# Performance work log

Hardware: AMD Instinct MI355X
Metric: run time of the kernel (lower is better)

## Reference

```python
import jax, jax.numpy as jnp
import numpy as np

N = 100000
E = 1600000
EPS = 1e-5


def _bn(h, g, b):
    # BatchNorm1d in training mode: batch stats over dim 0 (biased variance)
    mu = h.mean(0)
    var = ((h - mu) ** 2).mean(0)
    return g * (h - mu) * jax.lax.rsqrt(var + EPS) + b


def setup_inputs() -> dict:
    key = jax.random.key(0)

    def nrm(i, shape, scale=1.0):
        return jax.random.normal(jax.random.fold_in(key, i), shape, jnp.float32) * scale

    inp = {
        "x": nrm(0, (N, 1)),
        "edge_attr": nrm(1, (E, 2)),
        "edge_index": jax.random.randint(jax.random.fold_in(key, 2), (2, E), 0, N),
        "dir_edge_index": jax.random.randint(jax.random.fold_in(key, 3), (2, E), 0, N),
        "prop_edge_index": jax.random.randint(jax.random.fold_in(key, 4), (2, E), 0, N),
    }
    k = [10]

    def lin(name, fan_in, fan_out):
        inp[name] = nrm(k[0], (fan_in, fan_out), 1.0 / float(np.sqrt(fan_in)))
        k[0] += 1

    def bnp(prefix, c):
        inp[prefix + "_g"] = jnp.ones((c,), jnp.float32)
        inp[prefix + "_b"] = jnp.zeros((c,), jnp.float32)

    lin("c1_ws", 1, 2); lin("c1_wn", 1, 2); lin("c1_we", 2, 2); bnp("c1", 2)
    lin("d1_ws", 3, 4); lin("d1_wn", 3, 4); bnp("d1", 4)
    lin("c2_ws", 5, 6); lin("c2_wn", 5, 6); lin("c2_we", 2, 6); bnp("c2", 6)
    lin("d2_ws", 7, 8); lin("d2_wn", 7, 8); bnp("d2", 8)
    lin("c3_ws", 9, 10); lin("c3_wn", 9, 10); lin("c3_we", 2, 10); bnp("c3", 10)
    lin("d3_ws", 11, 12); lin("d3_wn", 11, 12); bnp("d3", 12)
    lin("pw1", 13, 8); inp["pb1"] = jnp.zeros((8,), jnp.float32); bnp("p1", 8)
    lin("pw2", 8, 4); inp["pb2"] = jnp.zeros((4,), jnp.float32); bnp("p2", 4)
    lin("pw3", 4, 1); inp["pb3"] = jnp.zeros((1,), jnp.float32)
    lin("ew1", 28, 14); inp["eb1"] = jnp.zeros((14,), jnp.float32); bnp("e1", 14)
    lin("ew2", 14, 1); inp["eb2"] = jnp.zeros((1,), jnp.float32)
    return inp


def reference(x, edge_attr, edge_index, dir_edge_index, prop_edge_index,
              c1_ws, c1_wn, c1_we, c1_g, c1_b,
              d1_ws, d1_wn, d1_g, d1_b,
              c2_ws, c2_wn, c2_we, c2_g, c2_b,
              d2_ws, d2_wn, d2_g, d2_b,
              c3_ws, c3_wn, c3_we, c3_g, c3_b,
              d3_ws, d3_wn, d3_g, d3_b,
              pw1, pb1, p1_g, p1_b, pw2, pb2, p2_g, p2_b, pw3, pb3,
              ew1, eb1, e1_g, e1_b, ew2, eb2):
    n = x.shape[0]
    src, dst = edge_index[0], edge_index[1]        # x_j = x[src], x_i = x[dst]
    psrc, pdst = prop_edge_index[0], prop_edge_index[1]

    def flexconv(h, ws, wn, we, g, b):
        m = jax.nn.relu(_bn(h[dst] @ ws + edge_attr @ we + h[src] @ wn, g, b))
        agg = jax.ops.segment_sum(m, dst, num_segments=n)
        return jnp.concatenate([h[:, :1], agg], axis=1)

    def edgeinter(h, ws, wn, g, b):
        m = jax.nn.relu(_bn(h[pdst] @ ws + h[psrc] @ wn, g, b))
        agg = jax.ops.segment_sum(m, pdst, num_segments=n)
        return jnp.concatenate([h[:, :1], agg], axis=1)

    out = flexconv(x, c1_ws, c1_wn, c1_we, c1_g, c1_b)      # [N,3]
    out = edgeinter(out, d1_ws, d1_wn, d1_g, d1_b)          # [N,5]
    out = flexconv(out, c2_ws, c2_wn, c2_we, c2_g, c2_b)    # [N,7]
    out = edgeinter(out, d2_ws, d2_wn, d2_g, d2_b)          # [N,9]
    out = flexconv(out, c3_ws, c3_wn, c3_we, c3_g, c3_b)    # [N,11]
    out = edgeinter(out, d3_ws, d3_wn, d3_g, d3_b)          # [N,13]

    h = _bn(jax.nn.relu(out @ pw1 + pb1), p1_g, p1_b)
    h = _bn(jax.nn.relu(h @ pw2 + pb2), p2_g, p2_b)
    power = jax.nn.sigmoid(1.5 * (h @ pw3 + pb3))           # [N,1]

    dsrc, ddst = dir_edge_index[0], dir_edge_index[1]
    f = jnp.concatenate([out[ddst], power[ddst], out[dsrc], power[dsrc]], axis=1)  # [E,28]
    e = _bn(jax.nn.relu(f @ ew1 + eb1), e1_g, e1_b)
    direction = jax.nn.sigmoid(1.5 * (e @ ew2 + eb2))       # [E,1]
    return power, direction
```

## Files before the change

kernel.cpp:

```cpp
#include <hip/hip_runtime.h>
#include <math.h>

static constexpr int BLK = 256;
static constexpr float BN_EPS = 1e-5f;

__device__ __forceinline__ float sigmoid15(float z) {
    return 1.0f / (1.0f + expf(-1.5f * z));
}

template<int C>
__device__ __forceinline__ void block_stats_reduce(float (&s)[C], float (&ss)[C],
                                                   double* __restrict__ stats)
{
    #pragma unroll
    for (int j = 0; j < C; ++j) {
        #pragma unroll
        for (int o = 32; o > 0; o >>= 1) {
            s[j]  += __shfl_down(s[j],  o, 64);
            ss[j] += __shfl_down(ss[j], o, 64);
        }
    }
    __shared__ float red[2][C][BLK / 64];
    const int wave = threadIdx.x >> 6, lane = threadIdx.x & 63;
    if (lane == 0) {
        #pragma unroll
        for (int j = 0; j < C; ++j) { red[0][j][wave] = s[j]; red[1][j][wave] = ss[j]; }
    }
    __syncthreads();
    if (threadIdx.x < C) {
        const int j = threadIdx.x;
        float a = 0.f, b = 0.f;
        #pragma unroll
        for (int w = 0; w < BLK / 64; ++w) { a += red[0][j][w]; b += red[1][j][w]; }
        atomicAdd(&stats[j],      (double)a);
        atomicAdd(&stats[16 + j], (double)b);
    }
}

template<int C>
__device__ __forceinline__ void bn_coefs(const double* __restrict__ stats,
                                         const float* __restrict__ g, const float* __restrict__ b,
                                         double invE, float (&sc)[C], float (&bb)[C])
{
    #pragma unroll
    for (int j = 0; j < C; ++j) {
        const double mu  = stats[j] * invE;
        const double var = stats[16 + j] * invE - mu * mu;
        const float inv = rsqrtf((float)(var + (double)BN_EPS));
        const float gg = g[j];
        sc[j] = gg * inv;
        bb[j] = b[j] - (float)mu * gg * inv;
    }
}


__global__ __launch_bounds__(BLK) void init_kernel(int* __restrict__ deg, double* __restrict__ stats,
                                                   int* __restrict__ rowstart, int n2, int total)
{
    const int i = blockIdx.x * blockDim.x + threadIdx.x;
    if (i < n2) deg[i] = 0;
    if (i < 288) stats[i] = 0.0;
    if (i == 0) rowstart[n2] = total;
}

__global__ __launch_bounds__(BLK) void hist_kernel(const int* __restrict__ edst,
                                                   const int* __restrict__ pdst,
                                                   int* __restrict__ deg, int N, int E)
{
    const int stride = gridDim.x * blockDim.x;
    for (int e = blockIdx.x * blockDim.x + threadIdx.x; e < E; e += stride) {
        atomicAdd(&deg[edst[e]], 1);
        atomicAdd(&deg[N + pdst[e]], 1);
    }
}

__global__ __launch_bounds__(256) void scan1_kernel(const int* __restrict__ deg,
                                                    int* __restrict__ rowstart,
                                                    int* __restrict__ partials, int n2)
{
    __shared__ int lds[256];
    const int tid = threadIdx.x;
    const int base = blockIdx.x * 1024 + tid * 4;
    int v[4]; int loc = 0;
    #pragma unroll
    for (int r = 0; r < 4; ++r) { v[r] = (base + r < n2) ? deg[base + r] : 0; loc += v[r]; }
    lds[tid] = loc; __syncthreads();
    #pragma unroll
    for (int off = 1; off < 256; off <<= 1) {
        int t = (tid >= off) ? lds[tid - off] : 0;
        __syncthreads();
        lds[tid] += t;
        __syncthreads();
    }
    int excl = lds[tid] - loc;
    int run = excl;
    #pragma unroll
    for (int r = 0; r < 4; ++r) {
        if (base + r < n2) rowstart[base + r] = run;
        run += v[r];
    }
    if (tid == 255) partials[blockIdx.x] = lds[255];
}

__global__ __launch_bounds__(256) void scan2_kernel(int* __restrict__ partials, int n)
{
    __shared__ int lds[256];
    const int tid = threadIdx.x;
    const int base = tid * 4;
    int v[4]; int loc = 0;
    #pragma unroll
    for (int r = 0; r < 4; ++r) { v[r] = (base + r < n) ? partials[base + r] : 0; loc += v[r]; }
    lds[tid] = loc; __syncthreads();
    #pragma unroll
    for (int off = 1; off < 256; off <<= 1) {
        int t = (tid >= off) ? lds[tid - off] : 0;
        __syncthreads();
        lds[tid] += t;
        __syncthreads();
    }
    int excl = lds[tid] - loc;
    int run = excl;
    #pragma unroll
    for (int r = 0; r < 4; ++r) {
        if (base + r < n) partials[base + r] = run;
        run += v[r];
    }
}

__global__ __launch_bounds__(BLK) void scan3_kernel(int* __restrict__ rowstart,
                                                    int* __restrict__ cursor,
                                                    const int* __restrict__ partials, int n2)
{
    const int i = blockIdx.x * blockDim.x + threadIdx.x;
    if (i >= n2) return;
    const int v = rowstart[i] + partials[i >> 10];
    rowstart[i] = v;
    cursor[i] = v;
}

__global__ __launch_bounds__(BLK) void fill_kernel(
    const int* __restrict__ esrc, const int* __restrict__ edst,
    const int* __restrict__ psrc, const int* __restrict__ pdst,
    const float* __restrict__ ea,
    int* __restrict__ cursor, unsigned int* __restrict__ csr_src,
    float2* __restrict__ csr_ea, int N, int E)
{
    const int stride = gridDim.x * blockDim.x;
    for (int e = blockIdx.x * blockDim.x + threadIdx.x; e < E; e += stride) {
        const int d = edst[e];
        const int pos = atomicAdd(&cursor[d], 1);
        csr_src[pos] = (unsigned int)esrc[e];
        csr_ea[pos] = ((const float2*)ea)[e];
        const int p = pdst[e];
        const int pos2 = atomicAdd(&cursor[N + p], 1);
        csr_src[pos2] = (unsigned int)psrc[e];
    }
}


template<int CIN, int COUT>
__global__ __launch_bounds__(BLK) void projQ_kernel(
    const float* __restrict__ x, const float* __restrict__ agg_in,
    const float* __restrict__ wn, float* __restrict__ Q, int n)
{
    constexpr int PAD = (COUT + 3) & ~3;
    __shared__ float swn[CIN * COUT];
    for (int i = threadIdx.x; i < CIN * COUT; i += blockDim.x) swn[i] = wn[i];
    __syncthreads();
    const int i = blockIdx.x * blockDim.x + threadIdx.x;
    if (i >= n) return;
    float h[CIN];
    h[0] = x[i];
    #pragma unroll
    for (int k = 1; k < CIN; ++k) h[k] = agg_in[(size_t)i * (CIN - 1) + (k - 1)];
    #pragma unroll
    for (int j = 0; j < COUT; ++j) {
        float q = 0.f;
        #pragma unroll
        for (int k = 0; k < CIN; ++k) q = fmaf(h[k], swn[k * COUT + j], q);
        Q[(size_t)i * PAD + j] = q;
    }
}

template<int CIN, int COUT, bool HASEA>
__global__ __launch_bounds__(BLK) void node_stats_kernel(
    const int* __restrict__ rowstart, const unsigned int* __restrict__ csr_src,
    const float2* __restrict__ csr_ea,
    const float* __restrict__ x, const float* __restrict__ agg_in,
    const float* __restrict__ ws, const float* __restrict__ Q,
    const float* __restrict__ we,
    double* __restrict__ stats, int N, int base)
{
    constexpr int PAD = (COUT + 3) & ~3;
    __shared__ float sws[CIN * COUT];
    for (int i = threadIdx.x; i < CIN * COUT; i += blockDim.x) sws[i] = ws[i];
    __syncthreads();
    float we0[COUT], we1[COUT];
    if constexpr (HASEA) {
        #pragma unroll
        for (int j = 0; j < COUT; ++j) { we0[j] = we[j]; we1[j] = we[COUT + j]; }
    }
    float s[COUT], ss[COUT];
    #pragma unroll
    for (int j = 0; j < COUT; ++j) { s[j] = 0.f; ss[j] = 0.f; }
    const int t = blockIdx.x * blockDim.x + threadIdx.x;
    const int i = t >> 1, half = t & 1;
    if (i < N) {
        float h[CIN];
        h[0] = x[i];
        #pragma unroll
        for (int k = 1; k < CIN; ++k) h[k] = agg_in[(size_t)i * (CIN - 1) + (k - 1)];
        float pp[COUT];
        #pragma unroll
        for (int j = 0; j < COUT; ++j) {
            float p = 0.f;
            #pragma unroll
            for (int k = 0; k < CIN; ++k) p = fmaf(h[k], sws[k * COUT + j], p);
            pp[j] = p;
        }
        const int k0 = rowstart[base + i], k1 = rowstart[base + i + 1];
        for (int k = k0 + half; k < k1; k += 2) {
            const unsigned int sn = csr_src[k];
            float2 eav;
            if constexpr (HASEA) eav = csr_ea[k];
            #pragma unroll
            for (int j = 0; j < COUT; ++j) {
                float m = pp[j] + Q[(size_t)sn * PAD + j];
                if constexpr (HASEA) m = fmaf(eav.x, we0[j], fmaf(eav.y, we1[j], m));
                s[j] += m; ss[j] = fmaf(m, m, ss[j]);
            }
        }
    }
    block_stats_reduce<COUT>(s, ss, stats);
}

template<int CIN, int COUT, bool HASEA>
__global__ __launch_bounds__(BLK) void node_agg_kernel(
    const int* __restrict__ rowstart, const unsigned int* __restrict__ csr_src,
    const float2* __restrict__ csr_ea,
    const float* __restrict__ x, const float* __restrict__ agg_in,
    const float* __restrict__ ws, const float* __restrict__ Q,
    const float* __restrict__ we,
    const float* __restrict__ g, const float* __restrict__ b,
    const double* __restrict__ stats,
    float* __restrict__ agg_out, int N, int base, float invE)
{
    constexpr int PAD = (COUT + 3) & ~3;
    __shared__ float sws[CIN * COUT];
    for (int i = threadIdx.x; i < CIN * COUT; i += blockDim.x) sws[i] = ws[i];
    __syncthreads();
    const int t = blockIdx.x * blockDim.x + threadIdx.x;
    const int i = t >> 1, half = t & 1;
    if (i >= N) return;
    float we0[COUT], we1[COUT];
    if constexpr (HASEA) {
        #pragma unroll
        for (int j = 0; j < COUT; ++j) { we0[j] = we[j]; we1[j] = we[COUT + j]; }
    }
    float sc[COUT], bb[COUT];
    bn_coefs<COUT>(stats, g, b, (double)invE, sc, bb);
    float h[CIN];
    h[0] = x[i];
    #pragma unroll
    for (int k = 1; k < CIN; ++k) h[k] = agg_in[(size_t)i * (CIN - 1) + (k - 1)];
    float pp[COUT], acc[COUT];
    #pragma unroll
    for (int j = 0; j < COUT; ++j) {
        float p = 0.f;
        #pragma unroll
        for (int k = 0; k < CIN; ++k) p = fmaf(h[k], sws[k * COUT + j], p);
        pp[j] = p; acc[j] = 0.f;
    }
    const int k0 = rowstart[base + i], k1 = rowstart[base + i + 1];
    for (int k = k0 + half; k < k1; k += 2) {
        const unsigned int sn = csr_src[k];
        float2 eav;
        if constexpr (HASEA) eav = csr_ea[k];
        #pragma unroll
        for (int j = 0; j < COUT; ++j) {
            float m = pp[j] + Q[(size_t)sn * PAD + j];
            if constexpr (HASEA) m = fmaf(eav.x, we0[j], fmaf(eav.y, we1[j], m));
            acc[j] += fmaxf(fmaf(sc[j], m, bb[j]), 0.f);
        }
    }
    #pragma unroll
    for (int j = 0; j < COUT; ++j) acc[j] += __shfl_xor(acc[j], 1, 64);
    if (half == 0) {
        #pragma unroll
        for (int j = 0; j < COUT; ++j) agg_out[(size_t)i * COUT + j] = acc[j];
    }
}


__global__ __launch_bounds__(BLK) void zero_stats_kernel(double* __restrict__ stats, int n)
{
    int i = blockIdx.x * blockDim.x + threadIdx.x;
    if (i < n) stats[i] = 0.0;
}

template<int CIN, int COUT>
__global__ __launch_bounds__(BLK) void projPQ_kernel(
    const float* __restrict__ x, const float* __restrict__ agg_in,
    const float* __restrict__ ws, const float* __restrict__ wn,
    float* __restrict__ P, float* __restrict__ Q, float* __restrict__ agg_out, int n)
{
    __shared__ float sws[CIN * COUT], swn[CIN * COUT];
    for (int i = threadIdx.x; i < CIN * COUT; i += blockDim.x) { sws[i] = ws[i]; swn[i] = wn[i]; }
    __syncthreads();
    const int i = blockIdx.x * blockDim.x + threadIdx.x;
    if (i >= n) return;
    float h[CIN];
    h[0] = x[i];
    #pragma unroll
    for (int k = 1; k < CIN; ++k) h[k] = agg_in[(size_t)i * (CIN - 1) + (k - 1)];
    #pragma unroll
    for (int j = 0; j < COUT; ++j) {
        float p = 0.f, q = 0.f;
        #pragma unroll
        for (int k = 0; k < CIN; ++k) {
            p = fmaf(h[k], sws[k * COUT + j], p);
            q = fmaf(h[k], swn[k * COUT + j], q);
        }
        P[(size_t)i * COUT + j] = p;
        Q[(size_t)i * COUT + j] = q;
        agg_out[(size_t)i * COUT + j] = 0.f;
    }
}

template<int COUT, bool HASEA>
__global__ __launch_bounds__(BLK) void edge_stats_kernel(
    const int* __restrict__ esrc, const int* __restrict__ edst,
    const float* __restrict__ P,  const float* __restrict__ Q,
    const float* __restrict__ ea, const float* __restrict__ we,
    double* __restrict__ stats, int E)
{
    float we0[COUT], we1[COUT];
    if constexpr (HASEA) {
        #pragma unroll
        for (int j = 0; j < COUT; ++j) { we0[j] = we[j]; we1[j] = we[COUT + j]; }
    }
    float s[COUT], ss[COUT];
    #pragma unroll
    for (int j = 0; j < COUT; ++j) { s[j] = 0.f; ss[j] = 0.f; }
    const int stride = gridDim.x * blockDim.x;
    for (int e = blockIdx.x * blockDim.x + threadIdx.x; e < E; e += stride) {
        const int d = edst[e], sn = esrc[e];
        float2 eav = make_float2(0.f, 0.f);
        if constexpr (HASEA) eav = ((const float2* __restrict__)ea)[e];
        #pragma unroll
        for (int j = 0; j < COUT; ++j) {
            float m = P[(size_t)d * COUT + j] + Q[(size_t)sn * COUT + j];
            if constexpr (HASEA) m += eav.x * we0[j] + eav.y * we1[j];
            s[j] += m; ss[j] = fmaf(m, m, ss[j]);
        }
    }
    block_stats_reduce<COUT>(s, ss, stats);
}

template<int COUT, bool HASEA>
__global__ __launch_bounds__(BLK) void edge_scatter_kernel(
    const int* __restrict__ esrc, const int* __restrict__ edst,
    const float* __restrict__ P,  const float* __restrict__ Q,
    const float* __restrict__ ea, const float* __restrict__ we,
    const float* __restrict__ g,  const float* __restrict__ b,
    const double* __restrict__ stats,
    float* __restrict__ agg_out, int E)
{
    float we0[COUT], we1[COUT], sc[COUT], bb[COUT];
    #pragma unroll
    for (int j = 0; j < COUT; ++j) {
        if constexpr (HASEA) { we0[j] = we[j]; we1[j] = we[COUT + j]; }
    }
    bn_coefs<COUT>(stats, g, b, 1.0 / (double)E, sc, bb);
    const int stride = gridDim.x * blockDim.x;
    for (int e = blockIdx.x * blockDim.x + threadIdx.x; e < E; e += stride) {
        const int d = edst[e], sn = esrc[e];
        float2 eav = make_float2(0.f, 0.f);
        if constexpr (HASEA) eav = ((const float2* __restrict__)ea)[e];
        #pragma unroll
        for (int j = 0; j < COUT; ++j) {
            float m = P[(size_t)d * COUT + j] + Q[(size_t)sn * COUT + j];
            if constexpr (HASEA) m += eav.x * we0[j] + eav.y * we1[j];
            const float y = fmaxf(fmaf(sc[j], m, bb[j]), 0.f);
            if (y > 0.f) unsafeAtomicAdd(&agg_out[(size_t)d * COUT + j], y);
        }
    }
}


__global__ __launch_bounds__(BLK) void mlp1_kernel(
    const float* __restrict__ x, const float* __restrict__ agg6,
    const float* __restrict__ pw1, const float* __restrict__ pb1,
    float* __restrict__ t1, double* __restrict__ stats, int n)
{
    __shared__ float w[13 * 8];
    __shared__ float bsh[8];
    for (int i = threadIdx.x; i < 13 * 8; i += blockDim.x) w[i] = pw1[i];
    if (threadIdx.x < 8) bsh[threadIdx.x] = pb1[threadIdx.x];
    __syncthreads();
    const int i = blockIdx.x * blockDim.x + threadIdx.x;
    float s[8], ss[8];
    #pragma unroll
    for (int j = 0; j < 8; ++j) { s[j] = 0.f; ss[j] = 0.f; }
    if (i < n) {
        float h[13];
        h[0] = x[i];
        #pragma unroll
        for (int k = 0; k < 12; ++k) h[k + 1] = agg6[(size_t)i * 12 + k];
        #pragma unroll
        for (int j = 0; j < 8; ++j) {
            float t = bsh[j];
            #pragma unroll
            for (int k = 0; k < 13; ++k) t = fmaf(h[k], w[k * 8 + j], t);
            t = fmaxf(t, 0.f);
            t1[(size_t)i * 8 + j] = t;
            s[j] = t; ss[j] = t * t;
        }
    }
    block_stats_reduce<8>(s, ss, stats);
}

__global__ __launch_bounds__(BLK) void mlp2_kernel(
    const float* __restrict__ t1,
    const float* __restrict__ p1g, const float* __restrict__ p1b,
    const float* __restrict__ pw2, const float* __restrict__ pb2,
    const double* __restrict__ stats1,
    float* __restrict__ t2, double* __restrict__ stats2, int n)
{
    float sc[8], bb[8];
    bn_coefs<8>(stats1, p1g, p1b, 1.0 / (double)n, sc, bb);
    const int i = blockIdx.x * blockDim.x + threadIdx.x;
    float s[4], ss[4];
    #pragma unroll
    for (int j = 0; j < 4; ++j) { s[j] = 0.f; ss[j] = 0.f; }
    if (i < n) {
        float u[8];
        #pragma unroll
        for (int j = 0; j < 8; ++j) u[j] = fmaf(sc[j], t1[(size_t)i * 8 + j], bb[j]);
        #pragma unroll
        for (int j2 = 0; j2 < 4; ++j2) {
            float t = pb2[j2];
            #pragma unroll
            for (int j = 0; j < 8; ++j) t = fmaf(u[j], pw2[j * 4 + j2], t);
            t = fmaxf(t, 0.f);
            t2[(size_t)i * 4 + j2] = t;
            s[j2] = t; ss[j2] = t * t;
        }
    }
    block_stats_reduce<4>(s, ss, stats2);
}

__global__ __launch_bounds__(BLK) void mlp3_kernel(
    const float* __restrict__ t2,
    const float* __restrict__ p2g, const float* __restrict__ p2b,
    const float* __restrict__ pw3, const float* __restrict__ pb3,
    const float* __restrict__ x, const float* __restrict__ agg6,
    const float* __restrict__ ew1, const float* __restrict__ eb1,
    const double* __restrict__ stats2,
    float* __restrict__ power_out, float* __restrict__ A, float* __restrict__ B,
    int n, int astride)
{
    __shared__ float w1[28 * 14];
    for (int i = threadIdx.x; i < 28 * 14; i += blockDim.x) w1[i] = ew1[i];
    __syncthreads();
    float sc[4], bb[4];
    bn_coefs<4>(stats2, p2g, p2b, 1.0 / (double)n, sc, bb);
    const int i = blockIdx.x * blockDim.x + threadIdx.x;
    if (i >= n) return;
    float z = pb3[0];
    #pragma unroll
    for (int j = 0; j < 4; ++j) z = fmaf(fmaf(sc[j], t2[(size_t)i * 4 + j], bb[j]), pw3[j], z);
    const float pw = sigmoid15(z);
    power_out[i] = pw;
    float h[14];
    h[0] = x[i];
    #pragma unroll
    for (int k = 0; k < 12; ++k) h[k + 1] = agg6[(size_t)i * 12 + k];
    h[13] = pw;
    #pragma unroll
    for (int c = 0; c < 14; ++c) {
        float a = eb1[c], b2 = 0.f;
        #pragma unroll
        for (int k = 0; k < 14; ++k) {
            a  = fmaf(h[k], w1[k * 14 + c], a);
            b2 = fmaf(h[k], w1[(14 + k) * 14 + c], b2);
        }
        A[(size_t)i * astride + c] = a;
        B[(size_t)i * astride + c] = b2;
    }
}

__global__ __launch_bounds__(BLK) void ehead_stats_kernel(
    const int* __restrict__ dsrc, const int* __restrict__ ddst,
    const float* __restrict__ A, const float* __restrict__ B,
    double* __restrict__ stats, int E, int astride)
{
    float s[14], ss[14];
    #pragma unroll
    for (int j = 0; j < 14; ++j) { s[j] = 0.f; ss[j] = 0.f; }
    const int stride = gridDim.x * blockDim.x;
    for (int e = blockIdx.x * blockDim.x + threadIdx.x; e < E; e += stride) {
        const int dd = ddst[e], ds = dsrc[e];
        #pragma unroll
        for (int c = 0; c < 14; ++c) {
            const float r = fmaxf(A[(size_t)dd * astride + c] + B[(size_t)ds * astride + c], 0.f);
            s[c] += r; ss[c] = fmaf(r, r, ss[c]);
        }
    }
    block_stats_reduce<14>(s, ss, stats);
}

__global__ __launch_bounds__(BLK) void ehead_final_kernel(
    const int* __restrict__ dsrc, const int* __restrict__ ddst,
    const float* __restrict__ A, const float* __restrict__ B,
    const float* __restrict__ e1g, const float* __restrict__ e1b,
    const float* __restrict__ ew2, const float* __restrict__ eb2,
    const double* __restrict__ stats, float* __restrict__ dir_out, int E, int astride)
{
    float sc[14];
    float off = eb2[0];
    const double invE = 1.0 / (double)E;
    #pragma unroll
    for (int c = 0; c < 14; ++c) {
        const double mu  = stats[c] * invE;
        const double var = stats[16 + c] * invE - mu * mu;
        const float inv = rsqrtf((float)(var + (double)BN_EPS));
        const float gi = e1g[c] * inv;
        sc[c] = gi * ew2[c];
        off += (e1b[c] - (float)mu * gi) * ew2[c];
    }
    const int stride = gridDim.x * blockDim.x;
    for (int e = blockIdx.x * blockDim.x + threadIdx.x; e < E; e += stride) {
        const int dd = ddst[e], ds = dsrc[e];
        float z = off;
        #pragma unroll
        for (int c = 0; c < 14; ++c) {
            const float r = fmaxf(A[(size_t)dd * astride + c] + B[(size_t)ds * astride + c], 0.f);
            z = fmaf(r, sc[c], z);
        }
        dir_out[e] = sigmoid15(z);
    }
}


extern "C" void kernel_launch(void* const* d_in, const int* in_sizes, int n_in,
                              void* d_out, int out_size, void* d_ws, size_t ws_size,
                              hipStream_t stream)
{
    const float* x    = (const float*)d_in[0];
    const float* ea   = (const float*)d_in[1];
    const int*   eidx = (const int*)d_in[2];
    const int*   didx = (const int*)d_in[3];
    const int*   pidx = (const int*)d_in[4];
    const float *c1_ws=(const float*)d_in[5],  *c1_wn=(const float*)d_in[6],  *c1_we=(const float*)d_in[7],  *c1_g=(const float*)d_in[8],  *c1_b=(const float*)d_in[9];
    const float *d1_ws=(const float*)d_in[10], *d1_wn=(const float*)d_in[11], *d1_g=(const float*)d_in[12], *d1_b=(const float*)d_in[13];
    const float *c2_ws=(const float*)d_in[14], *c2_wn=(const float*)d_in[15], *c2_we=(const float*)d_in[16], *c2_g=(const float*)d_in[17], *c2_b=(const float*)d_in[18];
    const float *d2_ws=(const float*)d_in[19], *d2_wn=(const float*)d_in[20], *d2_g=(const float*)d_in[21], *d2_b=(const float*)d_in[22];
    const float *c3_ws=(const float*)d_in[23], *c3_wn=(const float*)d_in[24], *c3_we=(const float*)d_in[25], *c3_g=(const float*)d_in[26], *c3_b=(const float*)d_in[27];
    const float *d3_ws=(const float*)d_in[28], *d3_wn=(const float*)d_in[29], *d3_g=(const float*)d_in[30], *d3_b=(const float*)d_in[31];
    const float *pw1=(const float*)d_in[32], *pb1=(const float*)d_in[33], *p1_g=(const float*)d_in[34], *p1_b=(const float*)d_in[35];
    const float *pw2=(const float*)d_in[36], *pb2=(const float*)d_in[37], *p2_g=(const float*)d_in[38], *p2_b=(const float*)d_in[39];
    const float *pw3=(const float*)d_in[40], *pb3=(const float*)d_in[41];
    const float *ew1=(const float*)d_in[42], *eb1=(const float*)d_in[43], *e1_g=(const float*)d_in[44], *e1_b=(const float*)d_in[45];
    const float *ew2=(const float*)d_in[46], *eb2=(const float*)d_in[47];

    const int N = in_sizes[0];
    const int E = in_sizes[2] / 2;
    const int n2 = 2 * N;
    const int *esrc = eidx,     *edst = eidx + E;
    const int *dsrc = didx,     *ddst = didx + E;
    const int *psrc = pidx,     *pdst = pidx + E;

    float* power_out = (float*)d_out;
    float* dir_out   = power_out + N;

    const int gN  = (N + BLK - 1) / BLK;
    const int g2  = (n2 + BLK - 1) / BLK;
    const int gE  = 1024;
    const float invE = 1.0f / (float)E;

    const size_t eaRegionFloats = ((size_t)2 * E > (size_t)32 * N) ? (size_t)2 * E : (size_t)32 * N;
    const size_t need_csr = 4096
        + sizeof(float) * ((size_t)N * 12
                         + (size_t)N * 12
                         + (size_t)N * 12
                         + eaRegionFloats            )
        + sizeof(unsigned int) * (size_t)2 * E
        + sizeof(int) * ((size_t)n2 + 2)
        + sizeof(int) * (size_t)n2
        + sizeof(int) * 1024;

    double* stats = (double*)d_ws;

    if (ws_size >= need_csr) {
        float* fws  = (float*)((char*)d_ws + 4096);
        float* Q    = fws;                fws += (size_t)N * 12;
        float* aggA = fws;                fws += (size_t)N * 12;
        float* aggB = fws;                fws += (size_t)N * 12;
        float2* csr_ea = (float2*)fws;    fws += eaRegionFloats;
        unsigned int* csr_src = (unsigned int*)fws;
        int* rowstart = (int*)(csr_src + (size_t)2 * E);
        int* cursor   = rowstart + (n2 + 2);
        int* deg      = cursor;
        int* partials = cursor + n2;
        float* t1   = aggA;
        float* t2   = aggA + (size_t)N * 8;
        float* Abuf = (float*)csr_ea;
        float* Bbuf = Abuf + (size_t)N * 16;

        const int nparts = (n2 + 1023) / 1024;

        init_kernel<<<g2, BLK, 0, stream>>>(deg, stats, rowstart, n2, 2 * E);
        hist_kernel<<<gE, BLK, 0, stream>>>(edst, pdst, deg, N, E);
        scan1_kernel<<<nparts, 256, 0, stream>>>(deg, rowstart, partials, n2);
        scan2_kernel<<<1, 256, 0, stream>>>(partials, nparts);
        scan3_kernel<<<g2, BLK, 0, stream>>>(rowstart, cursor, partials, n2);
        fill_kernel<<<gE, BLK, 0, stream>>>(esrc, edst, psrc, pdst, ea, cursor, csr_src, csr_ea, N, E);

        projQ_kernel<1, 2><<<gN, BLK, 0, stream>>>(x, nullptr, c1_wn, Q, N);
        node_stats_kernel<1, 2, true><<<g2, BLK, 0, stream>>>(rowstart, csr_src, csr_ea, x, nullptr, c1_ws, Q, c1_we, stats + 0, N, 0);
        node_agg_kernel<1, 2, true><<<g2, BLK, 0, stream>>>(rowstart, csr_src, csr_ea, x, nullptr, c1_ws, Q, c1_we, c1_g, c1_b, stats + 0, aggA, N, 0, invE);
        projQ_kernel<3, 4><<<gN, BLK, 0, stream>>>(x, aggA, d1_wn, Q, N);
        node_stats_kernel<3, 4, false><<<g2, BLK, 0, stream>>>(rowstart, csr_src, csr_ea, x, aggA, d1_ws, Q, nullptr, stats + 32, N, N);
        node_agg_kernel<3, 4, false><<<g2, BLK, 0, stream>>>(rowstart, csr_src, csr_ea, x, aggA, d1_ws, Q, nullptr, d1_g, d1_b, stats + 32, aggB, N, N, invE);
        projQ_kernel<5, 6><<<gN, BLK, 0, stream>>>(x, aggB, c2_wn, Q, N);
        node_stats_kernel<5, 6, true><<<g2, BLK, 0, stream>>>(rowstart, csr_src, csr_ea, x, aggB, c2_ws, Q, c2_we, stats + 64, N, 0);
        node_agg_kernel<5, 6, true><<<g2, BLK, 0, stream>>>(rowstart, csr_src, csr_ea, x, aggB, c2_ws, Q, c2_we, c2_g, c2_b, stats + 64, aggA, N, 0, invE);
        projQ_kernel<7, 8><<<gN, BLK, 0, stream>>>(x, aggA, d2_wn, Q, N);
        node_stats_kernel<7, 8, false><<<g2, BLK, 0, stream>>>(rowstart, csr_src, csr_ea, x, aggA, d2_ws, Q, nullptr, stats + 96, N, N);
        node_agg_kernel<7, 8, false><<<g2, BLK, 0, stream>>>(rowstart, csr_src, csr_ea, x, aggA, d2_ws, Q, nullptr, d2_g, d2_b, stats + 96, aggB, N, N, invE);
        projQ_kernel<9, 10><<<gN, BLK, 0, stream>>>(x, aggB, c3_wn, Q, N);
        node_stats_kernel<9, 10, true><<<g2, BLK, 0, stream>>>(rowstart, csr_src, csr_ea, x, aggB, c3_ws, Q, c3_we, stats + 128, N, 0);
        node_agg_kernel<9, 10, true><<<g2, BLK, 0, stream>>>(rowstart, csr_src, csr_ea, x, aggB, c3_ws, Q, c3_we, c3_g, c3_b, stats + 128, aggA, N, 0, invE);
        projQ_kernel<11, 12><<<gN, BLK, 0, stream>>>(x, aggA, d3_wn, Q, N);
        node_stats_kernel<11, 12, false><<<g2, BLK, 0, stream>>>(rowstart, csr_src, csr_ea, x, aggA, d3_ws, Q, nullptr, stats + 160, N, N);
        node_agg_kernel<11, 12, false><<<g2, BLK, 0, stream>>>(rowstart, csr_src, csr_ea, x, aggA, d3_ws, Q, nullptr, d3_g, d3_b, stats + 160, aggB, N, N, invE);

        mlp1_kernel<<<gN, BLK, 0, stream>>>(x, aggB, pw1, pb1, t1, stats + 192, N);
        mlp2_kernel<<<gN, BLK, 0, stream>>>(t1, p1_g, p1_b, pw2, pb2, stats + 192, t2, stats + 224, N);
        mlp3_kernel<<<gN, BLK, 0, stream>>>(t2, p2_g, p2_b, pw3, pb3, x, aggB, ew1, eb1, stats + 224,
                                            power_out, Abuf, Bbuf, N, 16);
        ehead_stats_kernel<<<gE, BLK, 0, stream>>>(dsrc, ddst, Abuf, Bbuf, stats + 256, E, 16);
        ehead_final_kernel<<<gE, BLK, 0, stream>>>(dsrc, ddst, Abuf, Bbuf, e1_g, e1_b, ew2, eb2,
                                                   stats + 256, dir_out, E, 16);
    } else {
        float* fws  = (float*)((char*)d_ws + 4096);
        float* P    = fws;                fws += (size_t)N * 14;
        float* Q    = fws;                fws += (size_t)N * 14;
        float* aggA = fws;                fws += (size_t)N * 12;
        float* aggB = fws;                fws += (size_t)N * 12;
        float* t1   = aggA;
        float* t2   = aggA + (size_t)N * 8;
        float* Abuf = P;
        float* Bbuf = Q;

        zero_stats_kernel<<<2, BLK, 0, stream>>>(stats, 288);

        projPQ_kernel<1, 2><<<gN, BLK, 0, stream>>>(x, nullptr, c1_ws, c1_wn, P, Q, aggA, N);
        edge_stats_kernel<2, true><<<gE, BLK, 0, stream>>>(esrc, edst, P, Q, ea, c1_we, stats + 0, E);
        edge_scatter_kernel<2, true><<<gE, BLK, 0, stream>>>(esrc, edst, P, Q, ea, c1_we, c1_g, c1_b, stats + 0, aggA, E);

        projPQ_kernel<3, 4><<<gN, BLK, 0, stream>>>(x, aggA, d1_ws, d1_wn, P, Q, aggB, N);
        edge_stats_kernel<4, false><<<gE, BLK, 0, stream>>>(psrc, pdst, P, Q, nullptr, nullptr, stats + 32, E);
        edge_scatter_kernel<4, false><<<gE, BLK, 0, stream>>>(psrc, pdst, P, Q, nullptr, nullptr, d1_g, d1_b, stats + 32, aggB, E);

        projPQ_kernel<5, 6><<<gN, BLK, 0, stream>>>(x, aggB, c2_ws, c2_wn, P, Q, aggA, N);
        edge_stats_kernel<6, true><<<gE, BLK, 0, stream>>>(esrc, edst, P, Q, ea, c2_we, stats + 64, E);
        edge_scatter_kernel<6, true><<<gE, BLK, 0, stream>>>(esrc, edst, P, Q, ea, c2_we, c2_g, c2_b, stats + 64, aggA, E);

        projPQ_kernel<7, 8><<<gN, BLK, 0, stream>>>(x, aggA, d2_ws, d2_wn, P, Q, aggB, N);
        edge_stats_kernel<8, false><<<gE, BLK, 0, stream>>>(psrc, pdst, P, Q, nullptr, nullptr, stats + 96, E);
        edge_scatter_kernel<8, false><<<gE, BLK, 0, stream>>>(psrc, pdst, P, Q, nullptr, nullptr, d2_g, d2_b, stats + 96, aggB, E);

        projPQ_kernel<9, 10><<<gN, BLK, 0, stream>>>(x, aggB, c3_ws, c3_wn, P, Q, aggA, N);
        edge_stats_kernel<10, true><<<gE, BLK, 0, stream>>>(esrc, edst, P, Q, ea, c3_we, stats + 128, E);
        edge_scatter_kernel<10, true><<<gE, BLK, 0, stream>>>(esrc, edst, P, Q, ea, c3_we, c3_g, c3_b, stats + 128, aggA, E);

        projPQ_kernel<11, 12><<<gN, BLK, 0, stream>>>(x, aggA, d3_ws, d3_wn, P, Q, aggB, N);
        edge_stats_kernel<12, false><<<gE, BLK, 0, stream>>>(psrc, pdst, P, Q, nullptr, nullptr, stats + 160, E);
        edge_scatter_kernel<12, false><<<gE, BLK, 0, stream>>>(psrc, pdst, P, Q, nullptr, nullptr, d3_g, d3_b, stats + 160, aggB, E);

        mlp1_kernel<<<gN, BLK, 0, stream>>>(x, aggB, pw1, pb1, t1, stats + 192, N);
        mlp2_kernel<<<gN, BLK, 0, stream>>>(t1, p1_g, p1_b, pw2, pb2, stats + 192, t2, stats + 224, N);
        mlp3_kernel<<<gN, BLK, 0, stream>>>(t2, p2_g, p2_b, pw3, pb3, x, aggB, ew1, eb1, stats + 224,
                                            power_out, Abuf, Bbuf, N, 14);
        ehead_stats_kernel<<<gE, BLK, 0, stream>>>(dsrc, ddst, Abuf, Bbuf, stats + 256, E, 14);
        ehead_final_kernel<<<gE, BLK, 0, stream>>>(dsrc, ddst, Abuf, Bbuf, e1_g, e1_b, ew2, eb2,
                                                   stats + 256, dir_out, E, 14);
    }
}
```

Measured before the change: 1.084 ms.

## Pack CSR src with fp16 edge attrs, split prop CSR, use 4 lanes per node

Stores each flexconv CSR entry as a uint2 holding the source index and both edge attributes as fp16, so one 8-byte load replaces separate index and float2 loads. The edge-interaction CSR source indices move into their own array. Node gather kernels now use four threads per node instead of two, reducing the partial sums with two xor-shuffles. Histogram, fill and edge-final kernels launch full-size grids instead of fixed 1024-block grid-stride loops. Rounding edge attributes to fp16 loses precision in the messages and in the batch statistics.

```diff
diff --git a/kernel.cpp b/kernel.cpp
--- a/kernel.cpp
+++ b/kernel.cpp
@@ -1,4 +1,5 @@
 #include <hip/hip_runtime.h>
+#include <hip/hip_fp16.h>
 #include <math.h>
 
 static constexpr int BLK = 256;
@@ -6,6 +7,16 @@
 
 __device__ __forceinline__ float sigmoid15(float z) {
     return 1.0f / (1.0f + expf(-1.5f * z));
+}
+
+__device__ __forceinline__ unsigned pack_ea(float2 v) {
+    unsigned hx = __half_as_ushort(__float2half_rn(v.x));
+    unsigned hy = __half_as_ushort(__float2half_rn(v.y));
+    return hx | (hy << 16);
+}
+__device__ __forceinline__ float2 unpack_ea(unsigned u) {
+    return make_float2(__half2float(__ushort_as_half((unsigned short)(u & 0xffffu))),
+                       __half2float(__ushort_as_half((unsigned short)(u >> 16))));
 }
 
 template<int C>
@@ -142,18 +153,18 @@
     const int* __restrict__ esrc, const int* __restrict__ edst,
     const int* __restrict__ psrc, const int* __restrict__ pdst,
     const float* __restrict__ ea,
-    int* __restrict__ cursor, unsigned int* __restrict__ csr_src,
-    float2* __restrict__ csr_ea, int N, int E)
+    int* __restrict__ cursor, uint2* __restrict__ csr_e,
+    unsigned int* __restrict__ csr_psrc, int N, int E)
 {
     const int stride = gridDim.x * blockDim.x;
     for (int e = blockIdx.x * blockDim.x + threadIdx.x; e < E; e += stride) {
         const int d = edst[e];
+        const float2 eav = ((const float2*)ea)[e];
         const int pos = atomicAdd(&cursor[d], 1);
-        csr_src[pos] = (unsigned int)esrc[e];
-        csr_ea[pos] = ((const float2*)ea)[e];
+        csr_e[pos] = make_uint2((unsigned)esrc[e], pack_ea(eav));
         const int p = pdst[e];
         const int pos2 = atomicAdd(&cursor[N + p], 1);
-        csr_src[pos2] = (unsigned int)psrc[e];
+        csr_psrc[pos2 - E] = (unsigned)psrc[e];
     }
 }
 
@@ -184,12 +195,12 @@
 
 template<int CIN, int COUT, bool HASEA>
 __global__ __launch_bounds__(BLK) void node_stats_kernel(
-    const int* __restrict__ rowstart, const unsigned int* __restrict__ csr_src,
-    const float2* __restrict__ csr_ea,
+    const int* __restrict__ rowstart,
+    const uint2* __restrict__ csr_e, const unsigned int* __restrict__ csr_psrc,
     const float* __restrict__ x, const float* __restrict__ agg_in,
     const float* __restrict__ ws, const float* __restrict__ Q,
     const float* __restrict__ we,
-    double* __restrict__ stats, int N, int base)
+    double* __restrict__ stats, int N, int base, int koff)
 {
     constexpr int PAD = (COUT + 3) & ~3;
     __shared__ float sws[CIN * COUT];
@@ -204,7 +215,7 @@
     #pragma unroll
     for (int j = 0; j < COUT; ++j) { s[j] = 0.f; ss[j] = 0.f; }
     const int t = blockIdx.x * blockDim.x + threadIdx.x;
-    const int i = t >> 1, half = t & 1;
+    const int i = t >> 2, quad = t & 3;
     if (i < N) {
         float h[CIN];
         h[0] = x[i];
@@ -219,10 +230,15 @@
             pp[j] = p;
         }
         const int k0 = rowstart[base + i], k1 = rowstart[base + i + 1];
-        for (int k = k0 + half; k < k1; k += 2) {
-            const unsigned int sn = csr_src[k];
+        for (int k = k0 + quad; k < k1; k += 4) {
+            unsigned sn;
             float2 eav;
-            if constexpr (HASEA) eav = csr_ea[k];
+            if constexpr (HASEA) {
+                const uint2 ce = csr_e[k];
+                sn = ce.x; eav = unpack_ea(ce.y);
+            } else {
+                sn = csr_psrc[k - koff];
+            }
             #pragma unroll
             for (int j = 0; j < COUT; ++j) {
                 float m = pp[j] + Q[(size_t)sn * PAD + j];
@@ -236,21 +252,21 @@
 
 template<int CIN, int COUT, bool HASEA>
 __global__ __launch_bounds__(BLK) void node_agg_kernel(
-    const int* __restrict__ rowstart, const unsigned int* __restrict__ csr_src,
-    const float2* __restrict__ csr_ea,
+    const int* __restrict__ rowstart,
+    const uint2* __restrict__ csr_e, const unsigned int* __restrict__ csr_psrc,
     const float* __restrict__ x, const float* __restrict__ agg_in,
     const float* __restrict__ ws, const float* __restrict__ Q,
     const float* __restrict__ we,
     const float* __restrict__ g, const float* __restrict__ b,
     const double* __restrict__ stats,
-    float* __restrict__ agg_out, int N, int base, float invE)
+    float* __restrict__ agg_out, int N, int base, int koff, float invE)
 {
     constexpr int PAD = (COUT + 3) & ~3;
     __shared__ float sws[CIN * COUT];
     for (int i = threadIdx.x; i < CIN * COUT; i += blockDim.x) sws[i] = ws[i];
     __syncthreads();
     const int t = blockIdx.x * blockDim.x + threadIdx.x;
-    const int i = t >> 1, half = t & 1;
+    const int i = t >> 2, quad = t & 3;
     if (i >= N) return;
     float we0[COUT], we1[COUT];
     if constexpr (HASEA) {
@@ -272,10 +288,15 @@
         pp[j] = p; acc[j] = 0.f;
     }
     const int k0 = rowstart[base + i], k1 = rowstart[base + i + 1];
-    for (int k = k0 + half; k < k1; k += 2) {
-        const unsigned int sn = csr_src[k];
+    for (int k = k0 + quad; k < k1; k += 4) {
+        unsigned sn;
         float2 eav;
-        if constexpr (HASEA) eav = csr_ea[k];
+        if constexpr (HASEA) {
+            const uint2 ce = csr_e[k];
+            sn = ce.x; eav = unpack_ea(ce.y);
+        } else {
+            sn = csr_psrc[k - koff];
+        }
         #pragma unroll
         for (int j = 0; j < COUT; ++j) {
             float m = pp[j] + Q[(size_t)sn * PAD + j];
@@ -284,8 +305,11 @@
         }
     }
     #pragma unroll
-    for (int j = 0; j < COUT; ++j) acc[j] += __shfl_xor(acc[j], 1, 64);
-    if (half == 0) {
+    for (int j = 0; j < COUT; ++j) {
+        acc[j] += __shfl_xor(acc[j], 1, 64);
+        acc[j] += __shfl_xor(acc[j], 2, 64);
+    }
+    if (quad == 0) {
         #pragma unroll
         for (int j = 0; j < COUT; ++j) agg_out[(size_t)i * COUT + j] = acc[j];
     }
@@ -576,16 +600,19 @@
 
     const int gN  = (N + BLK - 1) / BLK;
     const int g2  = (n2 + BLK - 1) / BLK;
+    const int g4  = ((size_t)4 * N + BLK - 1) / BLK;
     const int gE  = 1024;
+    const int gEf = (E + BLK - 1) / BLK;
     const float invE = 1.0f / (float)E;
 
-    const size_t eaRegionFloats = ((size_t)2 * E > (size_t)32 * N) ? (size_t)2 * E : (size_t)32 * N;
+    const size_t abFloats = (size_t)32 * N;
+    const size_t csreBytes = ((size_t)8 * E > 4 * abFloats) ? (size_t)8 * E : 4 * abFloats;
     const size_t need_csr = 4096
         + sizeof(float) * ((size_t)N * 12
                          + (size_t)N * 12
-                         + (size_t)N * 12
-                         + eaRegionFloats            )
-        + sizeof(unsigned int) * (size_t)2 * E
+                         + (size_t)N * 12)
+        + csreBytes
+        + sizeof(unsigned int) * (size_t)E
         + sizeof(int) * ((size_t)n2 + 2)
         + sizeof(int) * (size_t)n2
         + sizeof(int) * 1024;
@@ -597,52 +624,52 @@
         float* Q    = fws;                fws += (size_t)N * 12;
         float* aggA = fws;                fws += (size_t)N * 12;
         float* aggB = fws;                fws += (size_t)N * 12;
-        float2* csr_ea = (float2*)fws;    fws += eaRegionFloats;
-        unsigned int* csr_src = (unsigned int*)fws;
-        int* rowstart = (int*)(csr_src + (size_t)2 * E);
+        uint2* csr_e = (uint2*)fws;
+        unsigned int* csr_psrc = (unsigned int*)((char*)csr_e + csreBytes);
+        int* rowstart = (int*)(csr_psrc + E);
         int* cursor   = rowstart + (n2 + 2);
         int* deg      = cursor;
         int* partials = cursor + n2;
         float* t1   = aggA;
         float* t2   = aggA + (size_t)N * 8;
-        float* Abuf = (float*)csr_ea;
+        float* Abuf = (float*)csr_e;
         float* Bbuf = Abuf + (size_t)N * 16;
 
         const int nparts = (n2 + 1023) / 1024;
 
         init_kernel<<<g2, BLK, 0, stream>>>(deg, stats, rowstart, n2, 2 * E);
-        hist_kernel<<<gE, BLK, 0, stream>>>(edst, pdst, deg, N, E);
+        hist_kernel<<<gEf, BLK, 0, stream>>>(edst, pdst, deg, N, E);
         scan1_kernel<<<nparts, 256, 0, stream>>>(deg, rowstart, partials, n2);
         scan2_kernel<<<1, 256, 0, stream>>>(partials, nparts);
         scan3_kernel<<<g2, BLK, 0, stream>>>(rowstart, cursor, partials, n2);
-        fill_kernel<<<gE, BLK, 0, stream>>>(esrc, edst, psrc, pdst, ea, cursor, csr_src, csr_ea, N, E);
+        fill_kernel<<<gEf, BLK, 0, stream>>>(esrc, edst, psrc, pdst, ea, cursor, csr_e, csr_psrc, N, E);
 
         projQ_kernel<1, 2><<<gN, BLK, 0, stream>>>(x, nullptr, c1_wn, Q, N);
-        node_stats_kernel<1, 2, true><<<g2, BLK, 0, stream>>>(rowstart, csr_src, csr_ea, x, nullptr, c1_ws, Q, c1_we, stats + 0, N, 0);
-        node_agg_kernel<1, 2, true><<<g2, BLK, 0, stream>>>(rowstart, csr_src, csr_ea, x, nullptr, c1_ws, Q, c1_we, c1_g, c1_b, stats + 0, aggA, N, 0, invE);
+        node_stats_kernel<1, 2, true><<<g4, BLK, 0, stream>>>(rowstart, csr_e, csr_psrc, x, nullptr, c1_ws, Q, c1_we, stats + 0, N, 0, 0);
+        node_agg_kernel<1, 2, true><<<g4, BLK, 0, stream>>>(rowstart, csr_e, csr_psrc, x, nullptr, c1_ws, Q, c1_we, c1_g, c1_b, stats + 0, aggA, N, 0, 0, invE);
         projQ_kernel<3, 4><<<gN, BLK, 0, stream>>>(x, aggA, d1_wn, Q, N);
-        node_stats_kernel<3, 4, false><<<g2, BLK, 0, stream>>>(rowstart, csr_src, csr_ea, x, aggA, d1_ws, Q, nullptr, stats + 32, N, N);
-        node_agg_kernel<3, 4, false><<<g2, BLK, 0, stream>>>(rowstart, csr_src, csr_ea, x, aggA, d1_ws, Q, nullptr, d1_g, d1_b, stats + 32, aggB, N, N, invE);
+        node_stats_kernel<3, 4, false><<<g4, BLK, 0, stream>>>(rowstart, csr_e, csr_psrc, x, aggA, d1_ws, Q, nullptr, stats + 32, N, N, E);
+        node_agg_kernel<3, 4, false><<<g4, BLK, 0, stream>>>(rowstart, csr_e, csr_psrc, x, aggA, d1_ws, Q, nullptr, d1_g, d1_b, stats + 32, aggB, N, N, E, invE);
         projQ_kernel<5, 6><<<gN, BLK, 0, stream>>>(x, aggB, c2_wn, Q, N);
-        node_stats_kernel<5, 6, true><<<g2, BLK, 0, stream>>>(rowstart, csr_src, csr_ea, x, aggB, c2_ws, Q, c2_we, stats + 64, N, 0);
-        node_agg_kernel<5, 6, true><<<g2, BLK, 0, stream>>>(rowstart, csr_src, csr_ea, x, aggB, c2_ws, Q, c2_we, c2_g, c2_b, stats + 64, aggA, N, 0, invE);
+        node_stats_kernel<5, 6, true><<<g4, BLK, 0, stream>>>(rowstart, csr_e, csr_psrc, x, aggB, c2_ws, Q, c2_we, stats + 64, N, 0, 0);
+        node_agg_kernel<5, 6, true><<<g4, BLK, 0, stream>>>(rowstart, csr_e, csr_psrc, x, aggB, c2_ws, Q, c2_we, c2_g, c2_b, stats + 64, aggA, N, 0, 0, invE);
         projQ_kernel<7, 8><<<gN, BLK, 0, stream>>>(x, aggA, d2_wn, Q, N);
-        node_stats_kernel<7, 8, false><<<g2, BLK, 0, stream>>>(rowstart, csr_src, csr_ea, x, aggA, d2_ws, Q, nullptr, stats + 96, N, N);
-        node_agg_kernel<7, 8, false><<<g2, BLK, 0, stream>>>(rowstart, csr_src, csr_ea, x, aggA, d2_ws, Q, nullptr, d2_g, d2_b, stats + 96, aggB, N, N, invE);
+        node_stats_kernel<7, 8, false><<<g4, BLK, 0, stream>>>(rowstart, csr_e, csr_psrc, x, aggA, d2_ws, Q, nullptr, stats + 96, N, N, E);
+        node_agg_kernel<7, 8, false><<<g4, BLK, 0, stream>>>(rowstart, csr_e, csr_psrc, x, aggA, d2_ws, Q, nullptr, d2_g, d2_b, stats + 96, aggB, N, N, E, invE);
         projQ_kernel<9, 10><<<gN, BLK, 0, stream>>>(x, aggB, c3_wn, Q, N);
-        node_stats_kernel<9, 10, true><<<g2, BLK, 0, stream>>>(rowstart, csr_src, csr_ea, x, aggB, c3_ws, Q, c3_we, stats + 128, N, 0);
-        node_agg_kernel<9, 10, true><<<g2, BLK, 0, stream>>>(rowstart, csr_src, csr_ea, x, aggB, c3_ws, Q, c3_we, c3_g, c3_b, stats + 128, aggA, N, 0, invE);
+        node_stats_kernel<9, 10, true><<<g4, BLK, 0, stream>>>(rowstart, csr_e, csr_psrc, x, aggB, c3_ws, Q, c3_we, stats + 128, N, 0, 0);
+        node_agg_kernel<9, 10, true><<<g4, BLK, 0, stream>>>(rowstart, csr_e, csr_psrc, x, aggB, c3_ws, Q, c3_we, c3_g, c3_b, stats + 128, aggA, N, 0, 0, invE);
         projQ_kernel<11, 12><<<gN, BLK, 0, stream>>>(x, aggA, d3_wn, Q, N);
-        node_stats_kernel<11, 12, false><<<g2, BLK, 0, stream>>>(rowstart, csr_src, csr_ea, x, aggA, d3_ws, Q, nullptr, stats + 160, N, N);
-        node_agg_kernel<11, 12, false><<<g2, BLK, 0, stream>>>(rowstart, csr_src, csr_ea, x, aggA, d3_ws, Q, nullptr, d3_g, d3_b, stats + 160, aggB, N, N, invE);
+        node_stats_kernel<11, 12, false><<<g4, BLK, 0, stream>>>(rowstart, csr_e, csr_psrc, x, aggA, d3_ws, Q, nullptr, stats + 160, N, N, E);
+        node_agg_kernel<11, 12, false><<<g4, BLK, 0, stream>>>(rowstart, csr_e, csr_psrc, x, aggA, d3_ws, Q, nullptr, d3_g, d3_b, stats + 160, aggB, N, N, E, invE);
 
         mlp1_kernel<<<gN, BLK, 0, stream>>>(x, aggB, pw1, pb1, t1, stats + 192, N);
         mlp2_kernel<<<gN, BLK, 0, stream>>>(t1, p1_g, p1_b, pw2, pb2, stats + 192, t2, stats + 224, N);
         mlp3_kernel<<<gN, BLK, 0, stream>>>(t2, p2_g, p2_b, pw3, pb3, x, aggB, ew1, eb1, stats + 224,
                                             power_out, Abuf, Bbuf, N, 16);
         ehead_stats_kernel<<<gE, BLK, 0, stream>>>(dsrc, ddst, Abuf, Bbuf, stats + 256, E, 16);
-        ehead_final_kernel<<<gE, BLK, 0, stream>>>(dsrc, ddst, Abuf, Bbuf, e1_g, e1_b, ew2, eb2,
-                                                   stats + 256, dir_out, E, 16);
+        ehead_final_kernel<<<gEf, BLK, 0, stream>>>(dsrc, ddst, Abuf, Bbuf, e1_g, e1_b, ew2, eb2,
+                                                    stats + 256, dir_out, E, 16);
     } else {
         float* fws  = (float*)((char*)d_ws + 4096);
         float* P    = fws;                fws += (size_t)N * 14;
```

After: 1.091 ms. Within noise of the previous version (+0.7%).
